# Kernel tuning notes

Hardware: AMD Instinct MI355X
Metric: run time of the kernel (lower is better)

Reference implementation:

```python
import jax, jax.numpy as jnp
import numpy as np

B, T, C, H = 4, 2048, 1024, 16  # batch, seq, d_model, heads
D = C // H                      # head_dim = 64


def setup_inputs() -> dict:
    key = jax.random.key(0)
    ks = jax.random.split(key, 7)
    s = 1.0 / np.sqrt(C)
    return {
        "q_x": jax.random.normal(ks[0], (B, T, C), jnp.float32),
        "Wq": jax.random.normal(ks[1], (C, C), jnp.float32) * s,
        "bq": jax.random.normal(ks[2], (C,), jnp.float32) * 0.01,
        "Wk": jax.random.normal(ks[3], (C, C), jnp.float32) * s,
        "bk": jax.random.normal(ks[4], (C,), jnp.float32) * 0.01,
        "Wv": jax.random.normal(ks[5], (C, C), jnp.float32) * s,
        "bv": jax.random.normal(ks[6], (C,), jnp.float32) * 0.01,
    }


def reference(q_x, Wq, bq, Wk, bk, Wv, bv):
    # Self-attention path (k_x = v_x = q_x). Torch Linear: y = x @ W.T + b.
    q = q_x @ Wq.T + bq          # [B,T,C]
    k = q_x @ Wk.T + bk
    v = q_x @ Wv.T + bv
    # split heads: (B,T,C) -> (B,H,T,D); matches torch reshape(T,B*H,D) layout
    def heads(x):
        return x.reshape(B, T, H, D).transpose(0, 2, 1, 3)
    qh, kh, vh = heads(q), heads(k), heads(v)
    scale = 1.0 / np.sqrt(D)
    attn = jnp.einsum('bhtd,bhsd->bhts', qh, kh) * scale  # [B,H,T,T]
    attn = jax.nn.softmax(attn, axis=-1)
    x = jnp.einsum('bhts,bhsd->bhtd', attn, vh)           # [B,H,T,D]
    # merge heads back -> (B,T,C); batch_first=True output
    return x.transpose(0, 2, 1, 3).reshape(B, T, C)
```

## Files before the change

kernel.cpp:

```cpp
#include <hip/hip_runtime.h>
#include <hip/hip_bf16.h>
#include <stdint.h>
#include <stddef.h>

#define B_ 4
#define T_ 2048
#define C_ 1024
#define H_ 16
#define D_ 64
#define M_ (B_ * T_)

typedef __bf16 bf16x8 __attribute__((ext_vector_type(8)));
typedef _Float16 f16x8 __attribute__((ext_vector_type(8)));
typedef float  f32x4  __attribute__((ext_vector_type(4)));
typedef unsigned short u16x8 __attribute__((ext_vector_type(8)));
typedef unsigned short u16x4 __attribute__((ext_vector_type(4)));
typedef unsigned int   u32x4 __attribute__((ext_vector_type(4)));
typedef unsigned int   u32x2 __attribute__((ext_vector_type(2)));

__device__ __forceinline__ unsigned short f2bf(float f) {
    union { float f; unsigned int u; } c; c.f = f;
    unsigned int u = c.u;
    unsigned int r = (u + 0x7fffu + ((u >> 16) & 1u)) >> 16;
    return (unsigned short)r;
}

__device__ __forceinline__ unsigned int pkrtz(float a, float b) {
    return __builtin_bit_cast(unsigned int, __builtin_amdgcn_cvt_pkrtz(a, b));
}

__device__ __forceinline__ bf16x8 ld_bf16x8(const unsigned short* p) {
    u16x8 v = *(const u16x8*)p;
    return __builtin_bit_cast(bf16x8, v);
}

__device__ __forceinline__ f16x8 ld_f16x8(const unsigned short* p) {
    u16x8 v = *(const u16x8*)p;
    return __builtin_bit_cast(f16x8, v);
}

__device__ __forceinline__ void gl_lds16(const unsigned short* g, unsigned short* l) {
    __builtin_amdgcn_global_load_lds(
        (const void __attribute__((address_space(1)))*)g,
        (void __attribute__((address_space(3)))*)l, 16, 0, 0);
}

__device__ __forceinline__ f32x4 vmax4(f32x4 a, f32x4 b) {
    f32x4 r;
    r.x = fmaxf(a.x, b.x); r.y = fmaxf(a.y, b.y);
    r.z = fmaxf(a.z, b.z); r.w = fmaxf(a.w, b.w);
    return r;
}

#define X4_ ((int64_t)M_ * C_ / 4)
#define W4_ ((int64_t)C_ * C_ / 4)

__global__ __launch_bounds__(256)
void cvt_bf16(const float* __restrict__ x,
              const float* __restrict__ Wq, const float* __restrict__ Wk,
              const float* __restrict__ Wv,
              unsigned short* __restrict__ xb, unsigned short* __restrict__ wb)
{
    const int64_t i4 = (int64_t)blockIdx.x * blockDim.x + threadIdx.x;
    const float* src; unsigned short* dst; int64_t off;
    if (i4 < X4_) { src = x; dst = xb; off = i4; }
    else {
        int64_t j = i4 - X4_;
        int which = (int)(j / W4_);
        off = j - (int64_t)which * W4_;
        src = (which == 0) ? Wq : (which == 1) ? Wk : Wv;
        dst = wb + (int64_t)which * C_ * C_;
    }
    f32x4 v = *(const f32x4*)(src + off * 4);
    u16x4 o = { f2bf(v.x), f2bf(v.y), f2bf(v.z), f2bf(v.w) };
    *(u16x4*)(dst + off * 4) = o;
}

#define K1_ 0.180336880f

__global__ __launch_bounds__(256)
void qkv_gemm(const unsigned short* __restrict__ xb,
              const unsigned short* __restrict__ wb,
              const float* __restrict__ bq, const float* __restrict__ bk,
              const float* __restrict__ bv,
              unsigned short* __restrict__ qo,
              unsigned short* __restrict__ ko,
              unsigned short* __restrict__ vo)
{
    __shared__ alignas(16) unsigned short As[128 * 64];
    __shared__ alignas(16) unsigned short Bs[128 * 64];

    const int tid   = threadIdx.x;
    const int bm    = blockIdx.x;
    const int bn    = blockIdx.y;
    const int which = bn >> 3;
    const int n_base = (bn & 7) * 128;
    const int nrow   = bn * 128;
    const int m_base = bm * 128;

    const float* bias = (which == 0) ? bq : (which == 1) ? bk : bv;

    const int w = tid >> 6, lane = tid & 63;
    const int wr = w >> 1, wc = w & 1;
    const int ln = lane & 15, quad = lane >> 4;

    const int srow   = lane >> 3;
    const int schunk = (lane & 7) ^ srow;
    const int scu    = schunk * 8;

    const f32x4 fz = {0.f, 0.f, 0.f, 0.f};
    f32x4 acc[4][4];
#pragma unroll
    for (int i = 0; i < 4; ++i)
#pragma unroll
        for (int j = 0; j < 4; ++j) acc[i][j] = fz;

    for (int k0 = 0; k0 < C_; k0 += 64) {
        __syncthreads();
#pragma unroll
        for (int i = 0; i < 4; ++i) {
            const int r = w * 32 + i * 8 + srow;
            gl_lds16(xb + (size_t)(m_base + r) * C_ + k0 + scu, As + (w * 4 + i) * 512);
            gl_lds16(wb + (size_t)(nrow  + r) * C_ + k0 + scu, Bs + (w * 4 + i) * 512);
        }
        __syncthreads();

#pragma unroll
        for (int kk = 0; kk < 2; ++kk) {
            bf16x8 af[4], bfr[4];
#pragma unroll
            for (int mi = 0; mi < 4; ++mi) {
                const int r = wr * 64 + mi * 16 + ln;
                af[mi] = ld_bf16x8(&As[r * 64 + (((kk * 4 + quad) ^ (ln & 7)) * 8)]);
            }
#pragma unroll
            for (int ni = 0; ni < 4; ++ni) {
                const int r = wc * 64 + ni * 16 + ln;
                bfr[ni] = ld_bf16x8(&Bs[r * 64 + (((kk * 4 + quad) ^ (ln & 7)) * 8)]);
            }
#pragma unroll
            for (int mi = 0; mi < 4; ++mi)
#pragma unroll
                for (int ni = 0; ni < 4; ++ni)
                    acc[mi][ni] = __builtin_amdgcn_mfma_f32_16x16x32_bf16(
                        af[mi], bfr[ni], acc[mi][ni], 0, 0, 0);
        }
    }

#pragma unroll
    for (int ni = 0; ni < 4; ++ni) {
        const int n_local = n_base + wc * 64 + ni * 16 + ln;
        const float bv_ = bias[n_local];
        const int h = n_local >> 6, d = n_local & 63;
#pragma unroll
        for (int mi = 0; mi < 4; ++mi) {
            const int m0 = m_base + wr * 64 + mi * 16 + quad * 4;
            const int b  = m0 >> 11;
            const int t0 = m0 & (T_ - 1);
            f32x4 v = acc[mi][ni];
            if (which == 2) {
                const int tb   = t0 & ~127;
                const int w128 = t0 & 127;
                const int kvt  = w128 >> 4;
                const int qd   = (w128 >> 2) & 3;
                const int pos  = (kvt >> 1) * 32 + qd * 8 + (kvt & 1) * 4;
                u32x2 pk2 = { pkrtz(v.x + bv_, v.y + bv_),
                              pkrtz(v.z + bv_, v.w + bv_) };
                *(u32x2*)(&vo[((size_t)(b * H_ + h) * D_ + d) * T_ + tb + pos]) = pk2;
            } else if (which == 0) {
                unsigned short* dst =
                    qo + ((size_t)(b * H_ + h) * T_ + t0) * (size_t)D_ + d;
                dst[0 * D_] = f2bf((v.x + bv_) * K1_);
                dst[1 * D_] = f2bf((v.y + bv_) * K1_);
                dst[2 * D_] = f2bf((v.z + bv_) * K1_);
                dst[3 * D_] = f2bf((v.w + bv_) * K1_);
            } else {
                unsigned short* dst =
                    ko + ((size_t)(b * H_ + h) * T_ + t0) * (size_t)D_ + d;
                dst[0 * D_] = f2bf(v.x + bv_);
                dst[1 * D_] = f2bf(v.y + bv_);
                dst[2 * D_] = f2bf(v.z + bv_);
                dst[3 * D_] = f2bf(v.w + bv_);
            }
        }
    }
}

__global__ __launch_bounds__(256, 2)
void flash_attn(const unsigned short* __restrict__ qb,
                const unsigned short* __restrict__ kb,
                const unsigned short* __restrict__ vtb,
                float* __restrict__ out)
{
    __shared__ alignas(16) unsigned char smem[49152];
    float* Os = (float*)smem;
    unsigned short* Vs = (unsigned short*)(smem + 32768);

    const int tid = threadIdx.x;
    const int qt  = blockIdx.x;
    const int bh  = blockIdx.y;
    const int b   = bh >> 4, h = bh & 15;

    const int w = tid >> 6, lane = tid & 63;
    const int ln = lane & 15, quad = lane >> 4;

    const unsigned short* Qb = qb  + (size_t)bh * T_ * D_;
    const unsigned short* Kb = kb  + (size_t)bh * T_ * D_;
    const unsigned short* Vb = vtb + (size_t)bh * D_ * T_;

    const int qrow0 = qt * 128 + w * 16 + ln;
    const bf16x8 qA0 = ld_bf16x8(&Qb[(size_t)qrow0 * D_ + quad * 8]);
    const bf16x8 qA1 = ld_bf16x8(&Qb[(size_t)qrow0 * D_ + 32 + quad * 8]);
    const bf16x8 qB0 = ld_bf16x8(&Qb[(size_t)(qrow0 + 64) * D_ + quad * 8]);
    const bf16x8 qB1 = ld_bf16x8(&Qb[(size_t)(qrow0 + 64) * D_ + 32 + quad * 8]);

    const int srow   = lane >> 3;
    const int schunk = (lane & 7) ^ srow;
    const int scu    = schunk * 8;
    const int vrow = lane >> 4;

    const f32x4 fz = {0.f, 0.f, 0.f, 0.f};
    float m2a = -3.0e38f, lia = 0.f;
    float m2b = -3.0e38f, lib = 0.f;
    f32x4 accA[4], accB[4];
#pragma unroll
    for (int dt = 0; dt < 4; ++dt) { accA[dt] = fz; accB[dt] = fz; }

    auto stageK = [&](int kv0, int buf) {
        unsigned short* Ks = (unsigned short*)(smem + buf * 16384);
#pragma unroll
        for (int i = 0; i < 4; ++i) {
            const int kr = kv0 + w * 32 + i * 8 + srow;
            gl_lds16(Kb + (size_t)kr * D_ + scu, Ks + (w * 4 + i) * 512);
        }
    };
    auto stageV = [&](int kv0) {
#pragma unroll
        for (int i = 0; i < 4; ++i) {
            const int dr = (w * 4 + i) * 4 + vrow;
            const int vcs = (lane & 15) ^ ((i & 1) * 4 + vrow);
            gl_lds16(Vb + (size_t)dr * T_ + kv0 + vcs * 8, Vs + (w * 4 + i) * 512);
        }
    };

    stageK(0, 0);

    for (int kv0 = 0; kv0 < T_; kv0 += 128) {
        const int cur = (kv0 >> 7) & 1;
        __syncthreads();
        stageV(kv0);
        if (kv0 + 128 < T_) stageK(kv0 + 128, cur ^ 1);

        const unsigned short* Ks = (const unsigned short*)(smem + cur * 16384);

        f32x4 sA[8], sB[8];
#pragma unroll
        for (int kvt = 0; kvt < 8; ++kvt) {
            const int r_ = kvt * 16 + ln;
            bf16x8 kf0 = ld_bf16x8(&Ks[r_ * 64 + ((quad)     ^ (ln & 7)) * 8]);
            bf16x8 kf1 = ld_bf16x8(&Ks[r_ * 64 + ((quad + 4) ^ (ln & 7)) * 8]);
            f32x4 cA = fz, cB = fz;
            cA = __builtin_amdgcn_mfma_f32_16x16x32_bf16(kf0, qA0, cA, 0, 0, 0);
            cB = __builtin_amdgcn_mfma_f32_16x16x32_bf16(kf0, qB0, cB, 0, 0, 0);
            cA = __builtin_amdgcn_mfma_f32_16x16x32_bf16(kf1, qA1, cA, 0, 0, 0);
            cB = __builtin_amdgcn_mfma_f32_16x16x32_bf16(kf1, qB1, cB, 0, 0, 0);
            sA[kvt] = cA; sB[kvt] = cB;
        }

        u32x4 pksA[4], pksB[4];
        float alA, alB;
        bool growA, growB;
        {
            f32x4 mm = vmax4(vmax4(vmax4(sA[0], sA[1]), vmax4(sA[2], sA[3])),
                             vmax4(vmax4(sA[4], sA[5]), vmax4(sA[6], sA[7])));
            float mx = fmaxf(fmaxf(mm.x, mm.y), fmaxf(mm.z, mm.w));
            mx = fmaxf(mx, __shfl_xor(mx, 16));
            mx = fmaxf(mx, __shfl_xor(mx, 32));
            growA = __any(mx > m2a);
            const float nm = fmaxf(m2a, mx);
            alA = growA ? __builtin_amdgcn_exp2f(m2a - nm) : 1.0f;
            m2a = nm;
            f32x4 rsv = fz;
#pragma unroll
            for (int p = 0; p < 4; ++p) {
                f32x4 e0, e1;
                e0.x = __builtin_amdgcn_exp2f(sA[2*p].x - m2a);
                e0.y = __builtin_amdgcn_exp2f(sA[2*p].y - m2a);
                e0.z = __builtin_amdgcn_exp2f(sA[2*p].z - m2a);
                e0.w = __builtin_amdgcn_exp2f(sA[2*p].w - m2a);
                e1.x = __builtin_amdgcn_exp2f(sA[2*p+1].x - m2a);
                e1.y = __builtin_amdgcn_exp2f(sA[2*p+1].y - m2a);
                e1.z = __builtin_amdgcn_exp2f(sA[2*p+1].z - m2a);
                e1.w = __builtin_amdgcn_exp2f(sA[2*p+1].w - m2a);
                rsv += e0; rsv += e1;
                pksA[p][0] = pkrtz(e0.x, e0.y);
                pksA[p][1] = pkrtz(e0.z, e0.w);
                pksA[p][2] = pkrtz(e1.x, e1.y);
                pksA[p][3] = pkrtz(e1.z, e1.w);
            }
            float rs = (rsv.x + rsv.y) + (rsv.z + rsv.w);
            rs += __shfl_xor(rs, 16);
            rs += __shfl_xor(rs, 32);
            lia = lia * alA + rs;
        }
        {
            f32x4 mm = vmax4(vmax4(vmax4(sB[0], sB[1]), vmax4(sB[2], sB[3])),
                             vmax4(vmax4(sB[4], sB[5]), vmax4(sB[6], sB[7])));
            float mx = fmaxf(fmaxf(mm.x, mm.y), fmaxf(mm.z, mm.w));
            mx = fmaxf(mx, __shfl_xor(mx, 16));
            mx = fmaxf(mx, __shfl_xor(mx, 32));
            growB = __any(mx > m2b);
            const float nm = fmaxf(m2b, mx);
            alB = growB ? __builtin_amdgcn_exp2f(m2b - nm) : 1.0f;
            m2b = nm;
            f32x4 rsv = fz;
#pragma unroll
            for (int p = 0; p < 4; ++p) {
                f32x4 e0, e1;
                e0.x = __builtin_amdgcn_exp2f(sB[2*p].x - m2b);
                e0.y = __builtin_amdgcn_exp2f(sB[2*p].y - m2b);
                e0.z = __builtin_amdgcn_exp2f(sB[2*p].z - m2b);
                e0.w = __builtin_amdgcn_exp2f(sB[2*p].w - m2b);
                e1.x = __builtin_amdgcn_exp2f(sB[2*p+1].x - m2b);
                e1.y = __builtin_amdgcn_exp2f(sB[2*p+1].y - m2b);
                e1.z = __builtin_amdgcn_exp2f(sB[2*p+1].z - m2b);
                e1.w = __builtin_amdgcn_exp2f(sB[2*p+1].w - m2b);
                rsv += e0; rsv += e1;
                pksB[p][0] = pkrtz(e0.x, e0.y);
                pksB[p][1] = pkrtz(e0.z, e0.w);
                pksB[p][2] = pkrtz(e1.x, e1.y);
                pksB[p][3] = pkrtz(e1.z, e1.w);
            }
            float rs = (rsv.x + rsv.y) + (rsv.z + rsv.w);
            rs += __shfl_xor(rs, 16);
            rs += __shfl_xor(rs, 32);
            lib = lib * alB + rs;
        }

        if (growA) {
#pragma unroll
            for (int dt = 0; dt < 4; ++dt) accA[dt] *= alA;
        }
        if (growB) {
#pragma unroll
            for (int dt = 0; dt < 4; ++dt) accB[dt] *= alB;
        }

        __syncthreads();

#pragma unroll
        for (int dt = 0; dt < 4; ++dt) {
            const int vr = dt * 16 + ln;
#pragma unroll
            for (int p = 0; p < 4; ++p) {
                const int cl = ((p * 4 + quad) ^ (ln & 7));
                f16x8 vv = ld_f16x8(&Vs[vr * 128 + cl * 8]);
                accA[dt] = __builtin_amdgcn_mfma_f32_16x16x32_f16(
                    vv, __builtin_bit_cast(f16x8, pksA[p]), accA[dt], 0, 0, 0);
                accB[dt] = __builtin_amdgcn_mfma_f32_16x16x32_f16(
                    vv, __builtin_bit_cast(f16x8, pksB[p]), accB[dt], 0, 0, 0);
            }
        }
    }

    __syncthreads();
    const float rva = 1.0f / lia, rvb = 1.0f / lib;
#pragma unroll
    for (int dt = 0; dt < 4; ++dt)
#pragma unroll
        for (int r = 0; r < 4; ++r) {
            Os[(w * 16 + ln) * 72 + dt * 16 + quad * 4 + r]        = accA[dt][r] * rva;
            Os[(64 + w * 16 + ln) * 72 + dt * 16 + quad * 4 + r]   = accB[dt][r] * rvb;
        }
    __syncthreads();

    const int q  = tid >> 1;
    const int c0 = (tid & 1) * 32;
    const float* src = &Os[q * 72 + c0];
    float* dst = &out[((size_t)(b * T_ + qt * 128 + q)) * C_ + h * 64 + c0];
#pragma unroll
    for (int i = 0; i < 8; ++i)
        *(f32x4*)(dst + i * 4) = *(const f32x4*)(src + i * 4);
}

extern "C" void kernel_launch(void* const* d_in, const int* in_sizes, int n_in,
                              void* d_out, int out_size, void* d_ws, size_t ws_size,
                              hipStream_t stream) {
    const float* q_x = (const float*)d_in[0];
    const float* Wq  = (const float*)d_in[1];
    const float* bq  = (const float*)d_in[2];
    const float* Wk  = (const float*)d_in[3];
    const float* bk  = (const float*)d_in[4];
    const float* Wv  = (const float*)d_in[5];
    const float* bv  = (const float*)d_in[6];
    float* out = (float*)d_out;

    const size_t elems = (size_t)M_ * C_;
    unsigned short* xb  = (unsigned short*)d_ws;
    unsigned short* wb  = xb + elems;
    unsigned short* qb  = wb + (size_t)3 * C_ * C_;
    unsigned short* kb  = qb + elems;
    unsigned short* vtb = kb + elems;
    (void)ws_size; (void)in_sizes; (void)n_in; (void)out_size;

    const int64_t total4 = X4_ + 3 * W4_;
    cvt_bf16<<<(int)(total4 / 256), 256, 0, stream>>>(q_x, Wq, Wk, Wv, xb, wb);

    qkv_gemm<<<dim3(M_ / 128, 24), 256, 0, stream>>>(
        xb, wb, bq, bk, bv, qb, kb, vtb);

    flash_attn<<<dim3(T_ / 128, B_ * H_), 256, 0, stream>>>(qb, kb, vtb, out);
}
```

Baseline: 267.4 us.

## Use lazy softmax rescaling and compute row sums with an MFMA against ones

Each tile's exponentials are now computed against the running max from earlier tiles, starting from zero. The max is updated, and the accumulators rescaled, only when a row's max grows by more than 8 in log2 units. The per-tile VALU row-sum reduction and its cross-lane shuffles are replaced by an extra f16 MFMA that multiplies the packed probabilities by a ones vector. This cuts VALU and shuffle work in the softmax step, which competes with the MFMA pipeline. The trade-off is added matrix-core work and a risk of f16 overflow if scores jump sharply above the stale max, since the first tile is never guarded by a max computation.

```diff
diff --git a/kernel.cpp b/kernel.cpp
--- a/kernel.cpp
+++ b/kernel.cpp
@@ -220,11 +220,14 @@
     const int vrow = lane >> 4;
 
     const f32x4 fz = {0.f, 0.f, 0.f, 0.f};
-    float m2a = -3.0e38f, lia = 0.f;
-    float m2b = -3.0e38f, lib = 0.f;
+    float m2a = 0.f, m2b = 0.f;
     f32x4 accA[4], accB[4];
+    f32x4 acclA = fz, acclB = fz;
 #pragma unroll
     for (int dt = 0; dt < 4; ++dt) { accA[dt] = fz; accB[dt] = fz; }
+
+    const f16x8 ones = {(_Float16)1.f, (_Float16)1.f, (_Float16)1.f, (_Float16)1.f,
+                        (_Float16)1.f, (_Float16)1.f, (_Float16)1.f, (_Float16)1.f};
 
     auto stageK = [&](int kv0, int buf) {
         unsigned short* Ks = (unsigned short*)(smem + buf * 16384);
@@ -268,19 +271,9 @@
         }
 
         u32x4 pksA[4], pksB[4];
-        float alA, alB;
+        float flA = 1.0f, flB = 1.0f;
         bool growA, growB;
         {
-            f32x4 mm = vmax4(vmax4(vmax4(sA[0], sA[1]), vmax4(sA[2], sA[3])),
-                             vmax4(vmax4(sA[4], sA[5]), vmax4(sA[6], sA[7])));
-            float mx = fmaxf(fmaxf(mm.x, mm.y), fmaxf(mm.z, mm.w));
-            mx = fmaxf(mx, __shfl_xor(mx, 16));
-            mx = fmaxf(mx, __shfl_xor(mx, 32));
-            growA = __any(mx > m2a);
-            const float nm = fmaxf(m2a, mx);
-            alA = growA ? __builtin_amdgcn_exp2f(m2a - nm) : 1.0f;
-            m2a = nm;
-            f32x4 rsv = fz;
 #pragma unroll
             for (int p = 0; p < 4; ++p) {
                 f32x4 e0, e1;
@@ -292,28 +285,24 @@
                 e1.y = __builtin_amdgcn_exp2f(sA[2*p+1].y - m2a);
                 e1.z = __builtin_amdgcn_exp2f(sA[2*p+1].z - m2a);
                 e1.w = __builtin_amdgcn_exp2f(sA[2*p+1].w - m2a);
-                rsv += e0; rsv += e1;
                 pksA[p][0] = pkrtz(e0.x, e0.y);
                 pksA[p][1] = pkrtz(e0.z, e0.w);
                 pksA[p][2] = pkrtz(e1.x, e1.y);
                 pksA[p][3] = pkrtz(e1.z, e1.w);
             }
-            float rs = (rsv.x + rsv.y) + (rsv.z + rsv.w);
-            rs += __shfl_xor(rs, 16);
-            rs += __shfl_xor(rs, 32);
-            lia = lia * alA + rs;
-        }
-        {
-            f32x4 mm = vmax4(vmax4(vmax4(sB[0], sB[1]), vmax4(sB[2], sB[3])),
-                             vmax4(vmax4(sB[4], sB[5]), vmax4(sB[6], sB[7])));
+            f32x4 mm = vmax4(vmax4(vmax4(sA[0], sA[1]), vmax4(sA[2], sA[3])),
+                             vmax4(vmax4(sA[4], sA[5]), vmax4(sA[6], sA[7])));
             float mx = fmaxf(fmaxf(mm.x, mm.y), fmaxf(mm.z, mm.w));
             mx = fmaxf(mx, __shfl_xor(mx, 16));
             mx = fmaxf(mx, __shfl_xor(mx, 32));
-            growB = __any(mx > m2b);
-            const float nm = fmaxf(m2b, mx);
-            alB = growB ? __builtin_amdgcn_exp2f(m2b - nm) : 1.0f;
-            m2b = nm;
-            f32x4 rsv = fz;
+            growA = __any(mx > m2a + 8.0f);
+            if (growA) {
+                const float nm = fmaxf(m2a, mx);
+                flA = __builtin_amdgcn_exp2f(m2a - nm);
+                m2a = nm;
+            }
+        }
+        {
 #pragma unroll
             for (int p = 0; p < 4; ++p) {
                 f32x4 e0, e1;
@@ -325,25 +314,22 @@
                 e1.y = __builtin_amdgcn_exp2f(sB[2*p+1].y - m2b);
                 e1.z = __builtin_amdgcn_exp2f(sB[2*p+1].z - m2b);
                 e1.w = __builtin_amdgcn_exp2f(sB[2*p+1].w - m2b);
-                rsv += e0; rsv += e1;
                 pksB[p][0] = pkrtz(e0.x, e0.y);
                 pksB[p][1] = pkrtz(e0.z, e0.w);
                 pksB[p][2] = pkrtz(e1.x, e1.y);
                 pksB[p][3] = pkrtz(e1.z, e1.w);
             }
-            float rs = (rsv.x + rsv.y) + (rsv.z + rsv.w);
-            rs += __shfl_xor(rs, 16);
-            rs += __shfl_xor(rs, 32);
-            lib = lib * alB + rs;
-        }
-
-        if (growA) {
-#pragma unroll
-            for (int dt = 0; dt < 4; ++dt) accA[dt] *= alA;
-        }
-        if (growB) {
-#pragma unroll
-            for (int dt = 0; dt < 4; ++dt) accB[dt] *= alB;
+            f32x4 mm = vmax4(vmax4(vmax4(sB[0], sB[1]), vmax4(sB[2], sB[3])),
+                             vmax4(vmax4(sB[4], sB[5]), vmax4(sB[6], sB[7])));
+            float mx = fmaxf(fmaxf(mm.x, mm.y), fmaxf(mm.z, mm.w));
+            mx = fmaxf(mx, __shfl_xor(mx, 16));
+            mx = fmaxf(mx, __shfl_xor(mx, 32));
+            growB = __any(mx > m2b + 8.0f);
+            if (growB) {
+                const float nm = fmaxf(m2b, mx);
+                flB = __builtin_amdgcn_exp2f(m2b - nm);
+                m2b = nm;
+            }
         }
 
         __syncthreads();
@@ -361,10 +347,28 @@
                     vv, __builtin_bit_cast(f16x8, pksB[p]), accB[dt], 0, 0, 0);
             }
         }
+#pragma unroll
+        for (int p = 0; p < 4; ++p) {
+            acclA = __builtin_amdgcn_mfma_f32_16x16x32_f16(
+                ones, __builtin_bit_cast(f16x8, pksA[p]), acclA, 0, 0, 0);
+            acclB = __builtin_amdgcn_mfma_f32_16x16x32_f16(
+                ones, __builtin_bit_cast(f16x8, pksB[p]), acclB, 0, 0, 0);
+        }
+
+        if (growA) {
+#pragma unroll
+            for (int dt = 0; dt < 4; ++dt) accA[dt] *= flA;
+            acclA *= flA;
+        }
+        if (growB) {
+#pragma unroll
+            for (int dt = 0; dt < 4; ++dt) accB[dt] *= flB;
+            acclB *= flB;
+        }
     }
 
     __syncthreads();
-    const float rva = 1.0f / lia, rvb = 1.0f / lib;
+    const float rva = 1.0f / acclA[0], rvb = 1.0f / acclB[0];
 #pragma unroll
     for (int dt = 0; dt < 4; ++dt)
 #pragma unroll
```

New measurement: 252.5 us. 5.6% less time.
